# Optimization experiments

Measured on AMD Instinct MI355X. Metric: run time of the kernel, lower is better.

Reference implementation:

```python
import jax, jax.numpy as jnp
import numpy as np


def binarize(w):
    # sign-binarization with straight-through estimator (identity grad)
    return w + jax.lax.stop_gradient(jnp.sign(w) - w)


def setup_inputs() -> dict:
    key = jax.random.key(0)
    ks = jax.random.split(key, 9)
    B, D_IN, H, D_OUT = 524288, 196, 128, 10
    s_in = 1.0 / np.sqrt(D_IN)
    s_h = 1.0 / np.sqrt(H)
    return {
        "x": jax.random.normal(ks[0], (B, D_IN), dtype=jnp.float32),
        "W1": jax.random.uniform(ks[1], (H, D_IN), jnp.float32, -s_in, s_in),
        "b1": jax.random.uniform(ks[2], (H,), jnp.float32, -s_in, s_in),
        "W2": jax.random.uniform(ks[3], (H, H), jnp.float32, -s_h, s_h),
        "b2": jax.random.uniform(ks[4], (H,), jnp.float32, -s_h, s_h),
        "W3": jax.random.uniform(ks[5], (H, H), jnp.float32, -s_h, s_h),
        "b3": jax.random.uniform(ks[6], (H,), jnp.float32, -s_h, s_h),
        "W4": jax.random.uniform(ks[7], (D_OUT, H), jnp.float32, -s_h, s_h),
        "b4": jax.random.uniform(ks[8], (D_OUT,), jnp.float32, -s_h, s_h),
    }


def reference(x, W1, b1, W2, b2, W3, b3, W4, b4):
    # x: [B, 196] (already flat). Hidden layers use binarized weights + ReLU.
    h = jax.nn.relu(x @ binarize(W1).T + b1)   # [B, 128]
    h = jax.nn.relu(h @ binarize(W2).T + b2)   # [B, 128]
    h = jax.nn.relu(h @ binarize(W3).T + b3)   # [B, 128]
    return h @ W4.T + b4                        # [B, 10] (full-precision head)
```

## Files before the change

### kernel.cpp

```cpp
#include <hip/hip_runtime.h>
#include <cstdint>


typedef __attribute__((ext_vector_type(8))) short bf16x8;
typedef __attribute__((ext_vector_type(4))) float f32x4;

typedef unsigned short u16;
typedef unsigned int u32;

#define WS_W1 0
#define WS_W2 28672
#define WS_W3 45056
#define WS_W4 61440
#define WS_TOTAL 63488

__device__ __forceinline__ u32 bf16_rne(float x) {
  u32 u = __float_as_uint(x);
  return (u + 0x7FFFu + ((u >> 16) & 1u)) >> 16;
}

__device__ __forceinline__ u16 sign_bf16(float v) {
  return (v > 0.f) ? 0x3F80u : ((v < 0.f) ? 0xBF80u : 0u);
}

__device__ __forceinline__ int kperm_inv(int p) {
  return ((p & 31) >> 1) + ((p & 1) << 4) + ((p >> 5) << 5);
}

__global__ __launch_bounds__(256) void prep_kernel(
    const float* __restrict__ W1, const float* __restrict__ W2,
    const float* __restrict__ W3, const float* __restrict__ W4,
    u16* __restrict__ ws) {
  int idx = blockIdx.x * 256 + threadIdx.x;
  if (idx < WS_W2) {
    int n = idx / 224, k = idx - n * 224;
    float v = (k < 196) ? W1[n * 196 + k] : 0.f;
    ws[idx] = (k < 196) ? sign_bf16(v) : 0u;
  } else if (idx < WS_W3) {
    int j = idx - WS_W2; int n = j >> 7, p = j & 127;
    ws[idx] = sign_bf16(W2[(n << 7) + kperm_inv(p)]);
  } else if (idx < WS_W4) {
    int j = idx - WS_W3; int n = j >> 7, p = j & 127;
    ws[idx] = sign_bf16(W3[(n << 7) + kperm_inv(p)]);
  } else if (idx < WS_TOTAL) {
    int j = idx - WS_W4; int c = j >> 7, p = j & 127;
    ws[idx] = (c < 10) ? (u16)bf16_rne(W4[(c << 7) + kperm_inv(p)]) : 0u;
  }
}

template <int KP, int SSTR>
__device__ __forceinline__ void layer_fwd(
    const char* __restrict__ src, char* __restrict__ dst,
    const u16* __restrict__ Wp, const float* __restrict__ bias,
    int m, int q, int wr, int wc) {
  f32x4 acc[2][4];
#pragma unroll
  for (int rt = 0; rt < 2; ++rt)
#pragma unroll
    for (int ct = 0; ct < 4; ++ct)
      acc[rt][ct] = (f32x4){0.f, 0.f, 0.f, 0.f};

  const u16* wb = Wp + (wc * 64 + m) * KP + q * 8;
  const char* ab = src + (wr * 32 + m) * SSTR + q * 16;

#pragma unroll
  for (int ks = 0; ks < KP / 32; ++ks) {
    bf16x8 b[4];
#pragma unroll
    for (int ct = 0; ct < 4; ++ct)
      b[ct] = *(const bf16x8*)(wb + ct * 16 * KP + ks * 32);
#pragma unroll
    for (int rt = 0; rt < 2; ++rt) {
      bf16x8 a = *(const bf16x8*)(ab + rt * 16 * SSTR + ks * 64);
#pragma unroll
      for (int ct = 0; ct < 4; ++ct)
        acc[rt][ct] =
            __builtin_amdgcn_mfma_f32_16x16x32_bf16(a, b[ct], acc[rt][ct], 0, 0, 0);
    }
  }

#pragma unroll
  for (int rt = 0; rt < 2; ++rt) {
#pragma unroll
    for (int cp = 0; cp < 2; ++cp) {
      int g = wc * 2 + cp;
      float bi0 = bias[g * 32 + m];
      float bi1 = bias[g * 32 + 16 + m];
#pragma unroll
      for (int j = 0; j < 4; ++j) {
        float v0 = fmaxf(acc[rt][2 * cp][j] + bi0, 0.f);
        float v1 = fmaxf(acc[rt][2 * cp + 1][j] + bi1, 0.f);
        int row = wr * 32 + rt * 16 + q * 4 + j;
        *(u32*)(dst + row * 272 + m * 4 + g * 64) =
            bf16_rne(v0) | (bf16_rne(v1) << 16);
      }
    }
  }
}

__global__ __launch_bounds__(256, 2) void mlp_kernel(
    const float* __restrict__ x, const u16* __restrict__ ws,
    const float* __restrict__ b1, const float* __restrict__ b2,
    const float* __restrict__ b3, const float* __restrict__ b4,
    float* __restrict__ out) {
  __shared__ char smemA[64 * 448];
  __shared__ char smemB[64 * 272];

  const int tid = threadIdx.x;
  const int lane = tid & 63;
  const int wave = tid >> 6;
  const int m = lane & 15;
  const int q = lane >> 4;
  const int wr = wave >> 1, wc = wave & 1;
  const size_t rowbase = (size_t)blockIdx.x * 64;

  const float4* xsrc = (const float4*)(x + rowbase * 196);
#pragma unroll
  for (int it = 0; it < 13; ++it) {
    int i = it * 256 + tid;
    if (i < 3136) {
      float4 v = xsrc[i];
      int r = i / 49;
      int c4 = i - r * 49;
      u32 lo = bf16_rne(v.x) | (bf16_rne(v.y) << 16);
      u32 hi = bf16_rne(v.z) | (bf16_rne(v.w) << 16);
      *(uint2*)(smemA + r * 448 + c4 * 8) = make_uint2(lo, hi);
    }
  }
  for (int i = tid; i < 448; i += 256) {
    int r = i / 7, c = i - r * 7;
    *(uint2*)(smemA + r * 448 + 392 + c * 8) = make_uint2(0u, 0u);
  }
  __syncthreads();

  layer_fwd<224, 448>(smemA, smemB, ws + WS_W1, b1, m, q, wr, wc);
  __syncthreads();
  layer_fwd<128, 272>(smemB, smemA, ws + WS_W2, b2, m, q, wr, wc);
  __syncthreads();
  layer_fwd<128, 272>(smemA, smemB, ws + WS_W3, b3, m, q, wr, wc);
  __syncthreads();

  {
    const int rb = wave * 16;
    f32x4 acc = (f32x4){0.f, 0.f, 0.f, 0.f};
    const char* ab = smemB + (rb + m) * 272 + q * 16;
    const u16* wb = ws + WS_W4 + m * 128 + q * 8;
#pragma unroll
    for (int ks = 0; ks < 4; ++ks) {
      bf16x8 a = *(const bf16x8*)(ab + ks * 64);
      bf16x8 b = *(const bf16x8*)(wb + ks * 32);
      acc = __builtin_amdgcn_mfma_f32_16x16x32_bf16(a, b, acc, 0, 0, 0);
    }
    if (m < 10) {
      float bi = b4[m];
#pragma unroll
      for (int j = 0; j < 4; ++j) {
        size_t row = rowbase + rb + q * 4 + j;
        out[row * 10 + m] = acc[j] + bi;
      }
    }
  }
}

extern "C" void kernel_launch(void* const* d_in, const int* in_sizes, int n_in,
                              void* d_out, int out_size, void* d_ws, size_t ws_size,
                              hipStream_t stream) {
  const float* x  = (const float*)d_in[0];
  const float* W1 = (const float*)d_in[1];
  const float* b1 = (const float*)d_in[2];
  const float* W2 = (const float*)d_in[3];
  const float* b2 = (const float*)d_in[4];
  const float* W3 = (const float*)d_in[5];
  const float* b3 = (const float*)d_in[6];
  const float* W4 = (const float*)d_in[7];
  const float* b4 = (const float*)d_in[8];
  u16* ws = (u16*)d_ws;
  float* out = (float*)d_out;

  prep_kernel<<<248, 256, 0, stream>>>(W1, W2, W3, W4, ws);
  mlp_kernel<<<8192, 256, 0, stream>>>(x, ws, b1, b2, b3, b4, out);
}
```

Measured before the change: 684.2 us.

## Keep activations in registers via transposed MFMA chaining, drop shared memory

Computes the transposed product (weights as the A operand, activations as the B operand), so each layer's accumulator layout can be repacked directly into the next layer's B fragments in registers. This removes all LDS staging and block barriers, and x is loaded straight from global memory into bf16 fragments. Each wave now handles 32 rows independently. Bias is folded into the accumulator init, and conversion uses packed v_cvt_pk_bf16_f32. The K permutation of the weights is changed to match the new fragment layout. The cost is higher register pressure, and the x loads are uncoalesced (strided rows per lane), which may hurt memory efficiency on a bandwidth-bound workload.

```diff
diff --git a/kernel.cpp b/kernel.cpp
--- a/kernel.cpp
+++ b/kernel.cpp
@@ -23,8 +23,8 @@
   return (v > 0.f) ? 0x3F80u : ((v < 0.f) ? 0xBF80u : 0u);
 }
 
-__device__ __forceinline__ int kperm_inv(int p) {
-  return ((p & 31) >> 1) + ((p & 1) << 4) + ((p >> 5) << 5);
+__device__ __forceinline__ int kperm(int pos) {
+  return 32 * (pos >> 5) + 16 * ((pos >> 2) & 1) + 4 * ((pos >> 3) & 3) + (pos & 3);
 }
 
 __global__ __launch_bounds__(256) void prep_kernel(
@@ -34,130 +34,162 @@
   int idx = blockIdx.x * 256 + threadIdx.x;
   if (idx < WS_W2) {
     int n = idx / 224, k = idx - n * 224;
-    float v = (k < 196) ? W1[n * 196 + k] : 0.f;
-    ws[idx] = (k < 196) ? sign_bf16(v) : 0u;
+    ws[idx] = (k < 196) ? sign_bf16(W1[n * 196 + k]) : (u16)0;
   } else if (idx < WS_W3) {
     int j = idx - WS_W2; int n = j >> 7, p = j & 127;
-    ws[idx] = sign_bf16(W2[(n << 7) + kperm_inv(p)]);
+    ws[idx] = sign_bf16(W2[(n << 7) + kperm(p)]);
   } else if (idx < WS_W4) {
     int j = idx - WS_W3; int n = j >> 7, p = j & 127;
-    ws[idx] = sign_bf16(W3[(n << 7) + kperm_inv(p)]);
+    ws[idx] = sign_bf16(W3[(n << 7) + kperm(p)]);
   } else if (idx < WS_TOTAL) {
     int j = idx - WS_W4; int c = j >> 7, p = j & 127;
-    ws[idx] = (c < 10) ? (u16)bf16_rne(W4[(c << 7) + kperm_inv(p)]) : 0u;
-  }
-}
-
-template <int KP, int SSTR>
-__device__ __forceinline__ void layer_fwd(
-    const char* __restrict__ src, char* __restrict__ dst,
-    const u16* __restrict__ Wp, const float* __restrict__ bias,
-    int m, int q, int wr, int wc) {
-  f32x4 acc[2][4];
-#pragma unroll
-  for (int rt = 0; rt < 2; ++rt)
-#pragma unroll
-    for (int ct = 0; ct < 4; ++ct)
-      acc[rt][ct] = (f32x4){0.f, 0.f, 0.f, 0.f};
-
-  const u16* wb = Wp + (wc * 64 + m) * KP + q * 8;
-  const char* ab = src + (wr * 32 + m) * SSTR + q * 16;
-
-#pragma unroll
-  for (int ks = 0; ks < KP / 32; ++ks) {
-    bf16x8 b[4];
-#pragma unroll
-    for (int ct = 0; ct < 4; ++ct)
-      b[ct] = *(const bf16x8*)(wb + ct * 16 * KP + ks * 32);
-#pragma unroll
-    for (int rt = 0; rt < 2; ++rt) {
-      bf16x8 a = *(const bf16x8*)(ab + rt * 16 * SSTR + ks * 64);
-#pragma unroll
-      for (int ct = 0; ct < 4; ++ct)
-        acc[rt][ct] =
-            __builtin_amdgcn_mfma_f32_16x16x32_bf16(a, b[ct], acc[rt][ct], 0, 0, 0);
-    }
-  }
-
-#pragma unroll
-  for (int rt = 0; rt < 2; ++rt) {
-#pragma unroll
-    for (int cp = 0; cp < 2; ++cp) {
-      int g = wc * 2 + cp;
-      float bi0 = bias[g * 32 + m];
-      float bi1 = bias[g * 32 + 16 + m];
-#pragma unroll
-      for (int j = 0; j < 4; ++j) {
-        float v0 = fmaxf(acc[rt][2 * cp][j] + bi0, 0.f);
-        float v1 = fmaxf(acc[rt][2 * cp + 1][j] + bi1, 0.f);
-        int row = wr * 32 + rt * 16 + q * 4 + j;
-        *(u32*)(dst + row * 272 + m * 4 + g * 64) =
-            bf16_rne(v0) | (bf16_rne(v1) << 16);
-      }
-    }
-  }
-}
-
-__global__ __launch_bounds__(256, 2) void mlp_kernel(
+    ws[idx] = (c < 10) ? (u16)bf16_rne(W4[(c << 7) + kperm(p)]) : (u16)0;
+  }
+}
+
+union BFU { bf16x8 v; u32 w[4]; };
+
+__device__ __forceinline__ u32 cvtpk(float lo, float hi) {
+  u32 r;
+  asm("v_cvt_pk_bf16_f32 %0, %1, %2" : "=v"(r) : "v"(lo), "v"(hi));
+  return r;
+}
+__device__ __forceinline__ u32 cvtpk_relu(float lo, float hi) {
+  return cvtpk(fmaxf(lo, 0.f), fmaxf(hi, 0.f));
+}
+
+__device__ __forceinline__ void to_bfrag(const f32x4 acc[8], bf16x8 bf[4]) {
+#pragma unroll
+  for (int ks = 0; ks < 4; ++ks) {
+    BFU t;
+    t.w[0] = cvtpk_relu(acc[2 * ks][0], acc[2 * ks][1]);
+    t.w[1] = cvtpk_relu(acc[2 * ks][2], acc[2 * ks][3]);
+    t.w[2] = cvtpk_relu(acc[2 * ks + 1][0], acc[2 * ks + 1][1]);
+    t.w[3] = cvtpk_relu(acc[2 * ks + 1][2], acc[2 * ks + 1][3]);
+    bf[ks] = t.v;
+  }
+}
+
+__device__ __forceinline__ void layer128(const u16* __restrict__ wp,
+                                         const float* __restrict__ bias,
+                                         int m, int q,
+                                         const bf16x8 bf0[4], const bf16x8 bf1[4],
+                                         f32x4 acc0[8], f32x4 acc1[8]) {
+#pragma unroll
+  for (int mt = 0; mt < 8; ++mt) {
+    f32x4 bv = *(const f32x4*)(bias + mt * 16 + q * 4);
+    acc0[mt] = bv;
+    acc1[mt] = bv;
+  }
+  const u16* wb = wp + m * 128 + q * 8;
+#pragma unroll
+  for (int ks = 0; ks < 4; ++ks) {
+#pragma unroll
+    for (int mt = 0; mt < 8; ++mt) {
+      bf16x8 a = *(const bf16x8*)(wb + mt * (16 * 128) + ks * 32);
+      acc0[mt] = __builtin_amdgcn_mfma_f32_16x16x32_bf16(a, bf0[ks], acc0[mt], 0, 0, 0);
+      acc1[mt] = __builtin_amdgcn_mfma_f32_16x16x32_bf16(a, bf1[ks], acc1[mt], 0, 0, 0);
+    }
+  }
+}
+
+__global__ __launch_bounds__(256, 3) void mlp_kernel(
     const float* __restrict__ x, const u16* __restrict__ ws,
     const float* __restrict__ b1, const float* __restrict__ b2,
     const float* __restrict__ b3, const float* __restrict__ b4,
     float* __restrict__ out) {
-  __shared__ char smemA[64 * 448];
-  __shared__ char smemB[64 * 272];
-
   const int tid = threadIdx.x;
   const int lane = tid & 63;
   const int wave = tid >> 6;
   const int m = lane & 15;
   const int q = lane >> 4;
-  const int wr = wave >> 1, wc = wave & 1;
-  const size_t rowbase = (size_t)blockIdx.x * 64;
-
-  const float4* xsrc = (const float4*)(x + rowbase * 196);
-#pragma unroll
-  for (int it = 0; it < 13; ++it) {
-    int i = it * 256 + tid;
-    if (i < 3136) {
-      float4 v = xsrc[i];
-      int r = i / 49;
-      int c4 = i - r * 49;
-      u32 lo = bf16_rne(v.x) | (bf16_rne(v.y) << 16);
-      u32 hi = bf16_rne(v.z) | (bf16_rne(v.w) << 16);
-      *(uint2*)(smemA + r * 448 + c4 * 8) = make_uint2(lo, hi);
-    }
-  }
-  for (int i = tid; i < 448; i += 256) {
-    int r = i / 7, c = i - r * 7;
-    *(uint2*)(smemA + r * 448 + 392 + c * 8) = make_uint2(0u, 0u);
-  }
-  __syncthreads();
-
-  layer_fwd<224, 448>(smemA, smemB, ws + WS_W1, b1, m, q, wr, wc);
-  __syncthreads();
-  layer_fwd<128, 272>(smemB, smemA, ws + WS_W2, b2, m, q, wr, wc);
-  __syncthreads();
-  layer_fwd<128, 272>(smemA, smemB, ws + WS_W3, b3, m, q, wr, wc);
-  __syncthreads();
-
+  const size_t row0 = ((size_t)blockIdx.x * 4 + wave) * 32;
+
+  f32x4 acc0[8], acc1[8];
+
+#pragma unroll
+  for (int mt = 0; mt < 8; ++mt) {
+    f32x4 bv = *(const f32x4*)(b1 + mt * 16 + q * 4);
+    acc0[mt] = bv;
+    acc1[mt] = bv;
+  }
   {
-    const int rb = wave * 16;
-    f32x4 acc = (f32x4){0.f, 0.f, 0.f, 0.f};
-    const char* ab = smemB + (rb + m) * 272 + q * 16;
-    const u16* wb = ws + WS_W4 + m * 128 + q * 8;
+    const float* xr0 = x + (row0 + (size_t)m) * 196;
+    const float* xr1 = xr0 + 16 * 196;
+    const u16* w1 = ws + WS_W1 + m * 224 + q * 8;
+#pragma unroll
+    for (int ks = 0; ks < 7; ++ks) {
+      BFU xf0, xf1;
+      if (ks < 6) {
+        float4 a0 = *(const float4*)(xr0 + ks * 32 + q * 8);
+        float4 a1 = *(const float4*)(xr0 + ks * 32 + q * 8 + 4);
+        float4 c0 = *(const float4*)(xr1 + ks * 32 + q * 8);
+        float4 c1 = *(const float4*)(xr1 + ks * 32 + q * 8 + 4);
+        xf0.w[0] = cvtpk(a0.x, a0.y); xf0.w[1] = cvtpk(a0.z, a0.w);
+        xf0.w[2] = cvtpk(a1.x, a1.y); xf0.w[3] = cvtpk(a1.z, a1.w);
+        xf1.w[0] = cvtpk(c0.x, c0.y); xf1.w[1] = cvtpk(c0.z, c0.w);
+        xf1.w[2] = cvtpk(c1.x, c1.y); xf1.w[3] = cvtpk(c1.z, c1.w);
+      } else {
+        float4 a0 = make_float4(0.f, 0.f, 0.f, 0.f);
+        float4 c0 = a0;
+        if (q == 0) {
+          a0 = *(const float4*)(xr0 + 192);
+          c0 = *(const float4*)(xr1 + 192);
+        }
+        xf0.w[0] = cvtpk(a0.x, a0.y); xf0.w[1] = cvtpk(a0.z, a0.w);
+        xf0.w[2] = 0u; xf0.w[3] = 0u;
+        xf1.w[0] = cvtpk(c0.x, c0.y); xf1.w[1] = cvtpk(c0.z, c0.w);
+        xf1.w[2] = 0u; xf1.w[3] = 0u;
+      }
+#pragma unroll
+      for (int mt = 0; mt < 8; ++mt) {
+        bf16x8 a = *(const bf16x8*)(w1 + mt * (16 * 224) + ks * 32);
+        acc0[mt] = __builtin_amdgcn_mfma_f32_16x16x32_bf16(a, xf0.v, acc0[mt], 0, 0, 0);
+        acc1[mt] = __builtin_amdgcn_mfma_f32_16x16x32_bf16(a, xf1.v, acc1[mt], 0, 0, 0);
+      }
+    }
+  }
+
+  bf16x8 bf0[4], bf1[4];
+  to_bfrag(acc0, bf0);
+  to_bfrag(acc1, bf1);
+  layer128(ws + WS_W2, b2, m, q, bf0, bf1, acc0, acc1);
+  to_bfrag(acc0, bf0);
+  to_bfrag(acc1, bf1);
+  layer128(ws + WS_W3, b3, m, q, bf0, bf1, acc0, acc1);
+  to_bfrag(acc0, bf0);
+  to_bfrag(acc1, bf1);
+
+  f32x4 o0, o1;
+  {
+    float bvv[4];
+#pragma unroll
+    for (int jr = 0; jr < 4; ++jr) {
+      int n = q * 4 + jr;
+      bvv[jr] = (n < 10) ? b4[n] : 0.f;
+    }
+    o0 = (f32x4){bvv[0], bvv[1], bvv[2], bvv[3]};
+    o1 = o0;
+    const u16* w4 = ws + WS_W4 + m * 128 + q * 8;
 #pragma unroll
     for (int ks = 0; ks < 4; ++ks) {
-      bf16x8 a = *(const bf16x8*)(ab + ks * 64);
-      bf16x8 b = *(const bf16x8*)(wb + ks * 32);
-      acc = __builtin_amdgcn_mfma_f32_16x16x32_bf16(a, b, acc, 0, 0, 0);
-    }
-    if (m < 10) {
-      float bi = b4[m];
-#pragma unroll
-      for (int j = 0; j < 4; ++j) {
-        size_t row = rowbase + rb + q * 4 + j;
-        out[row * 10 + m] = acc[j] + bi;
-      }
+      bf16x8 a = *(const bf16x8*)(w4 + ks * 32);
+      o0 = __builtin_amdgcn_mfma_f32_16x16x32_bf16(a, bf0[ks], o0, 0, 0, 0);
+      o1 = __builtin_amdgcn_mfma_f32_16x16x32_bf16(a, bf1[ks], o1, 0, 0, 0);
+    }
+  }
+
+  {
+    float* r0 = out + (row0 + (size_t)m) * 10;
+    float* r1 = r0 + 16 * 10;
+    if (q < 2) {
+      *(float2*)(r0 + q * 4)     = make_float2(o0[0], o0[1]);
+      *(float2*)(r0 + q * 4 + 2) = make_float2(o0[2], o0[3]);
+      *(float2*)(r1 + q * 4)     = make_float2(o1[0], o1[1]);
+      *(float2*)(r1 + q * 4 + 2) = make_float2(o1[2], o1[3]);
+    } else if (q == 2) {
+      *(float2*)(r0 + 8) = make_float2(o0[0], o0[1]);
+      *(float2*)(r1 + 8) = make_float2(o1[0], o1[1]);
     }
   }
 }
@@ -178,5 +210,5 @@
   float* out = (float*)d_out;
 
   prep_kernel<<<248, 256, 0, stream>>>(W1, W2, W3, W4, ws);
-  mlp_kernel<<<8192, 256, 0, stream>>>(x, ws, b1, b2, b3, b4, out);
-}
+  mlp_kernel<<<4096, 256, 0, stream>>>(x, ws, b1, b2, b3, b4, out);
+}
```

New measurement: 772.2 us. 12.9% more time.
